# Kernel optimization log

Measured on AMD Instinct MI355X. Metric: run time of the kernel, lower is better.

## Reference

```python
import math
import jax, jax.numpy as jnp
import numpy as np

N_EMBD = 1024
N_HEAD = 16
B, T = 2, 2048
MASK_VALUE = -1000000.0


def setup_inputs() -> dict:
    key = jax.random.key(0)
    ks = jax.random.split(key, 10)
    s = 1.0 / math.sqrt(N_EMBD)
    x = jax.random.normal(ks[0], (B, T, N_EMBD), dtype=jnp.float32)
    # torch.nn.Linear weights are (out_features, in_features)
    Wq = jax.random.normal(ks[1], (N_EMBD, N_EMBD), dtype=jnp.float32) * s
    bq = jax.random.normal(ks[2], (N_EMBD,), dtype=jnp.float32) * s
    Wk = jax.random.normal(ks[3], (N_EMBD, N_EMBD), dtype=jnp.float32) * s
    bk = jax.random.normal(ks[4], (N_EMBD,), dtype=jnp.float32) * s
    Wv = jax.random.normal(ks[5], (N_EMBD, N_EMBD), dtype=jnp.float32) * s
    bv = jax.random.normal(ks[6], (N_EMBD,), dtype=jnp.float32) * s
    Wp = jax.random.normal(ks[7], (N_EMBD, N_EMBD), dtype=jnp.float32) * s
    bp = jax.random.normal(ks[8], (N_EMBD,), dtype=jnp.float32) * s
    # causal attn mask (B, T, T): 1 where attention allowed
    attn_mask = jnp.broadcast_to(
        jnp.tril(jnp.ones((T, T), dtype=jnp.int32))[None], (B, T, T))
    valid_input_mask = jnp.ones((B, T), dtype=jnp.int32)
    return {"x": x, "Wq": Wq, "bq": bq, "Wk": Wk, "bk": bk,
            "Wv": Wv, "bv": bv, "Wp": Wp, "bp": bp,
            "attn_mask": attn_mask, "valid_input_mask": valid_input_mask}


def reference(x, Wq, bq, Wk, bk, Wv, bv, Wp, bp, attn_mask, valid_input_mask):
    Bb, Tt, C = x.shape
    H = N_HEAD
    d = C // H
    # projections (torch Linear: x @ W.T + b), split into heads -> (B, H, T, d)
    def heads(y):
        return y.reshape(Bb, Tt, H, d).transpose(0, 2, 1, 3)
    q = heads(x @ Wq.T + bq)
    k = heads(x @ Wk.T + bk)
    v = heads(x @ Wv.T + bv)
    # attention scores (B, H, T, T)
    att = jnp.einsum('bhtd,bhsd->bhts', q, k) * (1.0 / math.sqrt(d))
    att = jnp.where(attn_mask[:, None, :, :] == 0, MASK_VALUE, att)
    att = jnp.where(valid_input_mask[:, None, None, :] == 0, MASK_VALUE, att)
    att = jax.nn.softmax(att, axis=-1)
    y = jnp.einsum('bhts,bhsd->bhtd', att, v)
    y = y.transpose(0, 2, 1, 3).reshape(Bb, Tt, C)
    return y @ Wp.T + bp
```

## Files before the change

### kernel.cpp

```cpp
#include <hip/hip_runtime.h>
#include <hip/hip_bf16.h>
#include <stdint.h>

typedef unsigned short u16;
typedef __attribute__((ext_vector_type(8))) short bf16x8;
typedef __attribute__((ext_vector_type(4))) float f32x4;

#define AS1 __attribute__((address_space(1)))
#define AS3 __attribute__((address_space(3)))

__device__ __forceinline__ void gload_lds16(const void* g, void* l) {
  __builtin_amdgcn_global_load_lds((const AS1 void*)g, (AS3 void*)l, 16, 0, 0);
}

__device__ __forceinline__ u16 f2bf(float f) {
  union { float f; uint32_t u; } v; v.f = f;
  uint32_t r = v.u + 0x7FFFu + ((v.u >> 16) & 1u);
  return (u16)(r >> 16);
}

__global__ void cvt_all(const float* __restrict__ x,
                        const float* __restrict__ w0, const float* __restrict__ w1,
                        const float* __restrict__ w2, const float* __restrict__ w3,
                        u16* __restrict__ x16, u16* __restrict__ w16) {
  int i = blockIdx.x * 256 + threadIdx.x;
  const float* src; u16* dst; int off;
  if (i < 1048576) { src = x; dst = x16; off = i; }
  else {
    int j = i - 1048576; int w = j >> 18; off = j & 262143;
    src = (w == 0) ? w0 : (w == 1) ? w1 : (w == 2) ? w2 : w3;
    dst = w16 + (size_t)w * 1048576;
  }
  float4 v = ((const float4*)src)[off];
  uint64_t pk = (uint64_t)f2bf(v.x) | ((uint64_t)f2bf(v.y) << 16) |
                ((uint64_t)f2bf(v.z) << 32) | ((uint64_t)f2bf(v.w) << 48);
  ((uint64_t*)dst)[off] = pk;
}

#define BM 128
#define BN 128

template<int MODE>
__global__ __launch_bounds__(256, 2)
void gemm_bt(const u16* __restrict__ A, const u16* __restrict__ Bw,
             const float* __restrict__ bias0, const float* __restrict__ bias1,
             const float* __restrict__ bias2, void* __restrict__ Out,
             u16* __restrict__ VtOut, int M, int N, int K)
{
  __shared__ __align__(16) u16 As[BM * 64];
  __shared__ __align__(16) u16 Bs[BN * 64];
  const int tid = threadIdx.x;
  const int lane = tid & 63, wid = tid >> 6;
  const int lr = lane & 15, lg = lane >> 4;
  const int id = blockIdx.x;
  const int cpx = gridDim.x >> 3;
  const int swz = (id & 7) * cpx + (id >> 3);
  const int z = swz >> 8;
  const int rem = swz & 255;
  const int m0 = (rem >> 3) * BM, n0 = (rem & 7) * BN;
  const u16* Bz = Bw + (size_t)z * N * K;
  const float* bias = (MODE == 0) ? (z == 0 ? bias0 : (z == 1 ? bias1 : bias2)) : bias0;
  const int wm = (wid >> 1) * 64, wn = (wid & 1) * 64;

  f32x4 acc[4][4] = {};

  for (int kt = 0; kt < K; kt += 64) {
    __syncthreads();
#pragma unroll
    for (int i = 0; i < 4; ++i) {
      int cb = (i * 4 + wid) * 64;
      int c = cb + lane;
      int row = c >> 3, kc = (c & 7) * 8;
      gload_lds16(A  + (size_t)(m0 + row) * K + kt + kc, (void*)&As[(size_t)cb * 8]);
      gload_lds16(Bz + (size_t)(n0 + row) * K + kt + kc, (void*)&Bs[(size_t)cb * 8]);
    }
    __syncthreads();

#pragma unroll
    for (int s = 0; s < 2; ++s) {
      bf16x8 af[4], bfr[4];
#pragma unroll
      for (int mf = 0; mf < 4; ++mf) af[mf]  = *(const bf16x8*)&As[(wm + mf * 16 + lr) * 64 + s * 32 + lg * 8];
#pragma unroll
      for (int nf = 0; nf < 4; ++nf) bfr[nf] = *(const bf16x8*)&Bs[(wn + nf * 16 + lr) * 64 + s * 32 + lg * 8];
#pragma unroll
      for (int mf = 0; mf < 4; ++mf)
#pragma unroll
        for (int nf = 0; nf < 4; ++nf)
          acc[mf][nf] = __builtin_amdgcn_mfma_f32_16x16x32_bf16(af[mf], bfr[nf], acc[mf][nf], 0, 0, 0);
    }
  }

  if (MODE == 0) {
    __syncthreads();
    u16* tb = (wid < 2 ? As : Bs) + (wid & 1) * 4096;
    if (z == 2) {
#pragma unroll
      for (int nf = 0; nf < 4; ++nf) {
        float bv = bias[n0 + wn + nf * 16 + lr];
#pragma unroll
        for (int mf = 0; mf < 4; ++mf)
#pragma unroll
          for (int r = 0; r < 4; ++r)
            tb[(nf * 16 + lr) * 64 + (mf * 16 + lg * 4 + r)] = f2bf(acc[mf][nf][r] + bv);
      }
      asm volatile("s_waitcnt lgkmcnt(0)" ::: "memory");
#pragma unroll
      for (int c = 0; c < 8; ++c) {
        int nl = c * 8 + (lane >> 3);
        int mc = lane & 7;
        bf16x8 vv = *(const bf16x8*)&tb[nl * 64 + mc * 8];
        int ng = n0 + wn + nl;
        int mg = m0 + wm + mc * 8;
        size_t addr = (((size_t)(mg >> 11) * 16 + (ng >> 6)) * 64 + (ng & 63)) * 2048 + (mg & 2047);
        *(bf16x8*)&VtOut[addr] = vv;
      }
    } else {
      float qs = (z == 0) ? 0.125f : 1.0f;
#pragma unroll
      for (int nf = 0; nf < 4; ++nf) {
        float bv = bias[n0 + wn + nf * 16 + lr];
#pragma unroll
        for (int mf = 0; mf < 4; ++mf)
#pragma unroll
          for (int r = 0; r < 4; ++r)
            tb[(mf * 16 + lg * 4 + r) * 64 + nf * 16 + lr] = f2bf((acc[mf][nf][r] + bv) * qs);
      }
      asm volatile("s_waitcnt lgkmcnt(0)" ::: "memory");
      u16* Oz = (u16*)Out + (size_t)z * 4194304;
#pragma unroll
      for (int c = 0; c < 8; ++c) {
        int ml = c * 8 + (lane >> 3);
        int nc = lane & 7;
        bf16x8 vv = *(const bf16x8*)&tb[ml * 64 + nc * 8];
        int mg = m0 + wm + ml;
        int ng = n0 + wn + nc * 8;
        size_t addr = ((size_t)(mg >> 11) * 16 + (ng >> 6)) * (size_t)(2048 * 64)
                    + (size_t)(mg & 2047) * 64 + (ng & 63);
        *(bf16x8*)&Oz[addr] = vv;
      }
    }
    return;
  }

#pragma unroll
  for (int nf = 0; nf < 4; ++nf) {
    float bv = bias[n0 + wn + nf * 16 + lr];
#pragma unroll
    for (int mf = 0; mf < 4; ++mf)
#pragma unroll
      for (int r = 0; r < 4; ++r) {
        int m = m0 + wm + mf * 16 + lg * 4 + r;
        int n = n0 + wn + nf * 16 + lr;
        ((float*)Out)[(size_t)m * N + n] = acc[mf][nf][r] + bv;
      }
  }
}

__global__ __launch_bounds__(512, 4)
void attn_fwd(const u16* __restrict__ q, const u16* __restrict__ k,
              const u16* __restrict__ vt, u16* __restrict__ y)
{
  __shared__ __align__(16) u16 Ks[128 * 64];
  __shared__ __align__(16) u16 Vs[64 * 128];
  __shared__ __align__(16) u16 Ps[8][16 * 136];
  const int tid = threadIdx.x, lane = tid & 63, wid = tid >> 6;
  const int lr = lane & 15, lg = lane >> 4;
  const int bx = blockIdx.x, by = blockIdx.y;
  const int r4 = (bx + by) & 15;
  const int qt = (by & 16) ? r4 : 15 - r4;
  const int q0 = qt * 128;
  const int bh = by;
  const u16* qg = q + (size_t)bh * 2048 * 64;
  const u16* kg = k + (size_t)bh * 2048 * 64;
  const u16* vg = vt + (size_t)bh * 64 * 2048;
  const int trow0 = q0 + wid * 16;
  const int tq = trow0 + lr;

  bf16x8 qa[2];
#pragma unroll
  for (int kk = 0; kk < 2; ++kk)
    qa[kk] = *(const bf16x8*)&qg[(size_t)(trow0 + lr) * 64 + kk * 32 + lg * 8];

  const int l8 = lane >> 3, s8 = lane & 7;
  const int kr0 = wid * 16 + l8;
  const int vd  = wid * 8 + l8;
  const u16* kld = kg + (size_t)kr0 * 64 + s8 * 8;
  const u16* vld = vg + (size_t)vd * 2048 + s8 * 8;
  u16* kst0 = &Ks[kr0 * 64 + (s8 ^ l8) * 8];
  u16* kst1 = &Ks[(kr0 + 8) * 64 + (s8 ^ l8) * 8];
  u16* vst0 = &Vs[vd * 128 + ((s8    ) ^ (vd & 7)) * 8];
  u16* vst1 = &Vs[vd * 128 + ((s8 + 8) ^ (vd & 7)) * 8];

  bf16x8 ldK0, ldK1, ldV0, ldV1;
  ldK0 = *(const bf16x8*)(kld);
  ldK1 = *(const bf16x8*)(kld + 8 * 64);
  ldV0 = *(const bf16x8*)(vld);
  ldV1 = *(const bf16x8*)(vld + 64);

  f32x4 oacc[4] = {};
  float mrun = -1e30f, lrun = 0.f;
  const int nk2 = qt + 1;
  const int xsl = lr & 7;

  for (int j = 0; j < nk2; ++j) {
    *(bf16x8*)kst0 = ldK0;  *(bf16x8*)kst1 = ldK1;
    *(bf16x8*)vst0 = ldV0;  *(bf16x8*)vst1 = ldV1;
    if (j + 1 < nk2) {
      const u16* kn = kld + (size_t)(j + 1) * 8192;
      const u16* vn = vld + (size_t)(j + 1) * 128;
      ldK0 = *(const bf16x8*)(kn);
      ldK1 = *(const bf16x8*)(kn + 8 * 64);
      ldV0 = *(const bf16x8*)(vn);
      ldV1 = *(const bf16x8*)(vn + 64);
    }
    asm volatile("s_waitcnt lgkmcnt(0)" ::: "memory");
    __builtin_amdgcn_s_barrier();

    f32x4 sacc[8] = {};
#pragma unroll
    for (int kk = 0; kk < 2; ++kk) {
#pragma unroll
      for (int h = 0; h < 2; ++h) {
        bf16x8 kb[4];
#pragma unroll
        for (int sf = 0; sf < 4; ++sf)
          kb[sf] = *(const bf16x8*)&Ks[((h * 4 + sf) * 16 + lr) * 64 + (((kk * 4 + lg) ^ xsl) * 8)];
#pragma unroll
        for (int sf = 0; sf < 4; ++sf)
          sacc[h * 4 + sf] = __builtin_amdgcn_mfma_f32_16x16x32_bf16(kb[sf], qa[kk], sacc[h * 4 + sf], 0, 0, 0);
      }
    }

    if (j == qt) {
#pragma unroll
      for (int sf = 0; sf < 8; ++sf)
#pragma unroll
        for (int r = 0; r < 4; ++r) {
          int s = j * 128 + sf * 16 + lg * 4 + r;
          if (s > tq) sacc[sf][r] = -1e30f;
        }
    }

    float m01 = fmaxf(fmaxf(fmaxf(sacc[0][0], sacc[0][1]), fmaxf(sacc[0][2], sacc[0][3])),
                      fmaxf(fmaxf(sacc[1][0], sacc[1][1]), fmaxf(sacc[1][2], sacc[1][3])));
    float m23 = fmaxf(fmaxf(fmaxf(sacc[2][0], sacc[2][1]), fmaxf(sacc[2][2], sacc[2][3])),
                      fmaxf(fmaxf(sacc[3][0], sacc[3][1]), fmaxf(sacc[3][2], sacc[3][3])));
    float m45 = fmaxf(fmaxf(fmaxf(sacc[4][0], sacc[4][1]), fmaxf(sacc[4][2], sacc[4][3])),
                      fmaxf(fmaxf(sacc[5][0], sacc[5][1]), fmaxf(sacc[5][2], sacc[5][3])));
    float m67 = fmaxf(fmaxf(fmaxf(sacc[6][0], sacc[6][1]), fmaxf(sacc[6][2], sacc[6][3])),
                      fmaxf(fmaxf(sacc[7][0], sacc[7][1]), fmaxf(sacc[7][2], sacc[7][3])));
    float mx = fmaxf(fmaxf(m01, m23), fmaxf(m45, m67));
    mx = fmaxf(mx, __shfl_xor(mx, 16));
    mx = fmaxf(mx, __shfl_xor(mx, 32));
    if (!__all(mx - mrun <= 8.0f)) {
      float mn = fmaxf(mrun, mx);
      float scn = __expf(mrun - mn);
      mrun = mn;
      lrun *= scn;
      float scr[4];
#pragma unroll
      for (int r = 0; r < 4; ++r) scr[r] = __shfl(scn, lg * 4 + r);
#pragma unroll
      for (int nf = 0; nf < 4; ++nf)
#pragma unroll
        for (int r = 0; r < 4; ++r) oacc[nf][r] *= scr[r];
    }
    float rs = 0.f;
#pragma unroll
    for (int sf = 0; sf < 8; ++sf)
#pragma unroll
      for (int r = 0; r < 4; ++r) {
        float p = __expf(sacc[sf][r] - mrun);
        sacc[sf][r] = p;
        rs += p;
      }
    rs += __shfl_xor(rs, 16);
    rs += __shfl_xor(rs, 32);
    lrun += rs;

#pragma unroll
    for (int sf = 0; sf < 8; ++sf) {
      union { ushort4 u; uint2 d; } pk_;
      pk_.u.x = f2bf(sacc[sf][0]); pk_.u.y = f2bf(sacc[sf][1]);
      pk_.u.z = f2bf(sacc[sf][2]); pk_.u.w = f2bf(sacc[sf][3]);
      *(uint2*)&Ps[wid][lr * 136 + sf * 16 + lg * 4] = pk_.d;
    }

#pragma unroll
    for (int kk = 0; kk < 4; ++kk) {
      bf16x8 pa = *(const bf16x8*)&Ps[wid][lr * 136 + kk * 32 + lg * 8];
      bf16x8 vb[4];
#pragma unroll
      for (int nf = 0; nf < 4; ++nf)
        vb[nf] = *(const bf16x8*)&Vs[(nf * 16 + lr) * 128 + (((kk * 4 + lg) ^ xsl) * 8)];
#pragma unroll
      for (int nf = 0; nf < 4; ++nf)
        oacc[nf] = __builtin_amdgcn_mfma_f32_16x16x32_bf16(pa, vb[nf], oacc[nf], 0, 0, 0);
    }

    asm volatile("s_waitcnt lgkmcnt(0)" ::: "memory");
    __builtin_amdgcn_s_barrier();
  }

  const int b = bh >> 4, h = bh & 15;
#pragma unroll
  for (int r = 0; r < 4; ++r) {
    float lshf = __shfl(lrun, lg * 4 + r);
    float inv = 1.f / lshf;
    int t = trow0 + lg * 4 + r;
#pragma unroll
    for (int nf = 0; nf < 4; ++nf) {
      int n = nf * 16 + lr;
      y[((size_t)b * 2048 + t) * 1024 + h * 64 + n] = f2bf(oacc[nf][r] * inv);
    }
  }
}

extern "C" void kernel_launch(void* const* d_in, const int* in_sizes, int n_in,
                              void* d_out, int out_size, void* d_ws, size_t ws_size,
                              hipStream_t stream) {
  const float* x  = (const float*)d_in[0];
  const float* Wq = (const float*)d_in[1];
  const float* bq = (const float*)d_in[2];
  const float* Wk = (const float*)d_in[3];
  const float* bk = (const float*)d_in[4];
  const float* Wv = (const float*)d_in[5];
  const float* bv = (const float*)d_in[6];
  const float* Wp = (const float*)d_in[7];
  const float* bp = (const float*)d_in[8];

  char* ws = (char*)d_ws;
  u16* x16  = (u16*)(ws + (size_t)0);
  u16* w16  = (u16*)(ws + ((size_t)8  << 20));
  u16* q16  = (u16*)(ws + ((size_t)16 << 20));
  u16* k16  = (u16*)(ws + ((size_t)24 << 20));
  u16* vt16 = (u16*)(ws + ((size_t)40 << 20));
  u16* y16  = x16;

  cvt_all<<<8192, 256, 0, stream>>>(x, Wq, Wk, Wv, Wp, x16, w16);
  gemm_bt<0><<<768, 256, 0, stream>>>(x16, w16, bq, bk, bv, (void*)q16, vt16, 4096, 1024, 1024);
  attn_fwd<<<dim3(16, 32), 512, 0, stream>>>(q16, k16, vt16, y16);
  gemm_bt<1><<<256, 256, 0, stream>>>(y16, w16 + 3 * 1048576, bp, bp, bp, d_out, (u16*)nullptr, 4096, 1024, 1024);
}
```

Measured before the change: 116.7 us.

## Double-buffer GEMM LDS tiles with async global-to-LDS prefetch two stages ahead

Turns the bf16 GEMM mainloop into a two-stage LDS pipeline. Tiles for iterations it+1 and it+2 are issued with global_load_lds while the current tile is consumed, with vmcnt-based waits and raw barriers replacing the full syncthreads pair. This is meant to hide global load latency behind MFMA work. In exchange it doubles LDS use to 64KB per block, which may hurt the intended 2 blocks/CU occupancy. The epilogue scratch pointer is also remapped onto the enlarged As buffer.

```diff
diff --git a/kernel.cpp b/kernel.cpp
--- a/kernel.cpp
+++ b/kernel.cpp
@@ -47,8 +47,8 @@
              const float* __restrict__ bias2, void* __restrict__ Out,
              u16* __restrict__ VtOut, int M, int N, int K)
 {
-  __shared__ __align__(16) u16 As[BM * 64];
-  __shared__ __align__(16) u16 Bs[BN * 64];
+  __shared__ __align__(16) u16 As[2][BM * 64];
+  __shared__ __align__(16) u16 Bs[2][BN * 64];
   const int tid = threadIdx.x;
   const int lane = tid & 63, wid = tid >> 6;
   const int lr = lane & 15, lg = lane >> 4;
@@ -61,39 +61,59 @@
   const u16* Bz = Bw + (size_t)z * N * K;
   const float* bias = (MODE == 0) ? (z == 0 ? bias0 : (z == 1 ? bias1 : bias2)) : bias0;
   const int wm = (wid >> 1) * 64, wn = (wid & 1) * 64;
+  const int nit = K >> 6;
+
+  const int row_ = (tid) >> 0;
+
+#define STAGE(it, buf) do {                                                     \
+    int kt_ = (it) * 64;                                                        \
+    _Pragma("unroll")                                                           \
+    for (int i_ = 0; i_ < 4; ++i_) {                                            \
+      int cb_ = (i_ * 4 + wid) * 64;                                            \
+      int c_ = cb_ + lane;                                                      \
+      int row2_ = c_ >> 3, kc_ = (c_ & 7) * 8;                                  \
+      gload_lds16(A  + (size_t)(m0 + row2_) * K + kt_ + kc_,                    \
+                  (void*)&As[buf][(size_t)cb_ * 8]);                            \
+      gload_lds16(Bz + (size_t)(n0 + row2_) * K + kt_ + kc_,                    \
+                  (void*)&Bs[buf][(size_t)cb_ * 8]);                            \
+    }                                                                           \
+  } while (0)
 
   f32x4 acc[4][4] = {};
 
-  for (int kt = 0; kt < K; kt += 64) {
-    __syncthreads();
-#pragma unroll
-    for (int i = 0; i < 4; ++i) {
-      int cb = (i * 4 + wid) * 64;
-      int c = cb + lane;
-      int row = c >> 3, kc = (c & 7) * 8;
-      gload_lds16(A  + (size_t)(m0 + row) * K + kt + kc, (void*)&As[(size_t)cb * 8]);
-      gload_lds16(Bz + (size_t)(n0 + row) * K + kt + kc, (void*)&Bs[(size_t)cb * 8]);
-    }
-    __syncthreads();
-
+  STAGE(0, 0);
+  STAGE(1, 1);
+
+  for (int it = 0; it < nit; ++it) {
+    if (it + 1 < nit) asm volatile("s_waitcnt vmcnt(8)" ::: "memory");
+    else              asm volatile("s_waitcnt vmcnt(0)" ::: "memory");
+    __builtin_amdgcn_s_barrier();
+
+    const u16* Ab = &As[it & 1][0];
+    const u16* Bb = &Bs[it & 1][0];
 #pragma unroll
     for (int s = 0; s < 2; ++s) {
       bf16x8 af[4], bfr[4];
 #pragma unroll
-      for (int mf = 0; mf < 4; ++mf) af[mf]  = *(const bf16x8*)&As[(wm + mf * 16 + lr) * 64 + s * 32 + lg * 8];
-#pragma unroll
-      for (int nf = 0; nf < 4; ++nf) bfr[nf] = *(const bf16x8*)&Bs[(wn + nf * 16 + lr) * 64 + s * 32 + lg * 8];
+      for (int mf = 0; mf < 4; ++mf) af[mf]  = *(const bf16x8*)&Ab[(wm + mf * 16 + lr) * 64 + s * 32 + lg * 8];
+#pragma unroll
+      for (int nf = 0; nf < 4; ++nf) bfr[nf] = *(const bf16x8*)&Bb[(wn + nf * 16 + lr) * 64 + s * 32 + lg * 8];
 #pragma unroll
       for (int mf = 0; mf < 4; ++mf)
 #pragma unroll
         for (int nf = 0; nf < 4; ++nf)
           acc[mf][nf] = __builtin_amdgcn_mfma_f32_16x16x32_bf16(af[mf], bfr[nf], acc[mf][nf], 0, 0, 0);
     }
-  }
+
+    asm volatile("s_waitcnt lgkmcnt(0)" ::: "memory");
+    __builtin_amdgcn_s_barrier();
+    if (it + 2 < nit) STAGE(it + 2, it & 1);
+  }
+#undef STAGE
 
   if (MODE == 0) {
     __syncthreads();
-    u16* tb = (wid < 2 ? As : Bs) + (wid & 1) * 4096;
+    u16* tb = &As[0][0] + wid * 4096;
     if (z == 2) {
 #pragma unroll
       for (int nf = 0; nf < 4; ++nf) {
```

Result: slower. 130.2 us (+11.6%).
